# Optimization experiments

Measured on AMD Instinct MI355X. Metric: run time of the kernel, lower is better.

The kernel has to match this reference:

```python
import jax, jax.numpy as jnp
import numpy as np

E = 1024  # embedding_dim
A = 1024  # attention_dim


def setup_inputs() -> dict:
    key = jax.random.key(0)
    k0, k1, k2, k3 = jax.random.split(key, 4)
    embedded = jax.random.normal(k0, (4, 4096, E), dtype=jnp.float32)
    # torch Linear weight is [out, in]; stored here as [in, out] for x @ W
    scale = 1.0 / np.sqrt(E)
    Wk = jax.random.uniform(k1, (E, A), dtype=jnp.float32, minval=-scale, maxval=scale)
    Wq = jax.random.uniform(k2, (E, A), dtype=jnp.float32, minval=-scale, maxval=scale)
    Wv = jax.random.uniform(k3, (E, A), dtype=jnp.float32, minval=-scale, maxval=scale)
    return {"embedded": embedded, "Wk": Wk, "Wq": Wq, "Wv": Wv}


def reference(embedded, Wk, Wq, Wv):
    B, T, C = embedded.shape
    K = embedded @ Wk  # [B,T,A]
    Q = embedded @ Wq
    V = embedded @ Wv
    d_k = Q.shape[-1]
    scores = jnp.einsum('bqa,bka->bqk', Q, K) / jnp.sqrt(jnp.float32(d_k))
    causal = jnp.tril(jnp.ones((T, T), dtype=bool))
    scores = jnp.where(causal, scores, -jnp.inf)
    attn = jax.nn.softmax(scores, axis=-1)
    out = jnp.einsum('bqk,bka->bqa', attn, V)
    return jnp.round(out, decimals=4)
```

## Files before the change

### kernel.cpp

```cpp
#include <hip/hip_runtime.h>
#include <hip/hip_fp16.h>

#define T_SEQ 4096
#define NBATCH 4
#define EDIM 1024
#define ADIM 1024
#define MTOT (NBATCH * T_SEQ)

typedef _Float16 f16x8 __attribute__((ext_vector_type(8)));
typedef float f32x4 __attribute__((ext_vector_type(4)));

#define STAGE(SRC, LD, LDSARR)                                               \
  {                                                                          \
    _Pragma("unroll") for (int t = 0; t < 2; ++t) {                          \
      const int rb = w * 2 + t;                                              \
      const _Float16* gsrc =                                                 \
          (SRC) + (size_t)(rb * 16 + (lane & 15)) * (LD) + (lane >> 4) * 8;  \
      __builtin_amdgcn_global_load_lds(                                      \
          (const __attribute__((address_space(1))) void*)gsrc,               \
          (__attribute__((address_space(3))) void*)&LDSARR[rb * 512], 16,    \
          0, 0);                                                             \
    }                                                                        \
  }

#define FRAG(LDSARR, B4, G) (*(const f16x8*)&LDSARR[((B4) * 4 + (G)) * 128 + lr * 8])

__global__ __launch_bounds__(256) void cast_x(const float* __restrict__ X,
                                              _Float16* __restrict__ Xh) {
  const size_t i = ((size_t)blockIdx.x * 256 + threadIdx.x) * 8;
  float4 a = ((const float4*)(X + i))[0];
  float4 b = ((const float4*)(X + i))[1];
  f16x8 o = {(_Float16)a.x, (_Float16)a.y, (_Float16)a.z, (_Float16)a.w,
             (_Float16)b.x, (_Float16)b.y, (_Float16)b.z, (_Float16)b.w};
  *(f16x8*)(Xh + i) = o;
}

__global__ __launch_bounds__(256) void cast_transpose_w(
    const float* __restrict__ Wk, const float* __restrict__ Wq,
    const float* __restrict__ Wv, _Float16* __restrict__ Wt) {
  __shared__ float tile[32][33];
  const int z = blockIdx.z;
  const float* W = (z == 0) ? Wk : (z == 1) ? Wq : Wv;
  const int n0 = blockIdx.x * 32, k0 = blockIdx.y * 32;
  const int tx = threadIdx.x, ty = threadIdx.y;
#pragma unroll
  for (int yy = 0; yy < 32; yy += 8)
    tile[ty + yy][tx] = W[(size_t)(k0 + ty + yy) * ADIM + n0 + tx];
  __syncthreads();
  _Float16* out = Wt + (size_t)z * EDIM * ADIM;
#pragma unroll
  for (int yy = 0; yy < 32; yy += 8)
    out[(size_t)(n0 + ty + yy) * EDIM + k0 + tx] = (_Float16)tile[tx][ty + yy];
}

__global__ __launch_bounds__(256) void gemm_qkv(
    const _Float16* __restrict__ Xh, const _Float16* __restrict__ Wt,
    _Float16* __restrict__ Qb, _Float16* __restrict__ Kb,
    _Float16* __restrict__ Vt) {
  const int z = blockIdx.z;
  const _Float16* Bt = Wt + (size_t)z * EDIM * ADIM;
  __shared__ __align__(16) _Float16 Al[4096];
  __shared__ __align__(16) _Float16 Bl[4096];
  const int tid = threadIdx.x;
  const int lane = tid & 63, w = tid >> 6;
  const int wm = w >> 1, wn = w & 1;
  const int lr = lane & 15, g = lane >> 4;
  const int h = blockIdx.y * gridDim.x + blockIdx.x;
  const int orig = (h & 7) * 128 + (h >> 3);
  const int m0 = (orig >> 3) * 128, n0 = (orig & 7) * 128;

  f32x4 acc[4][4] = {};

  for (int k0 = 0; k0 < EDIM; k0 += 32) {
    STAGE(Xh + (size_t)m0 * EDIM + k0, EDIM, Al);
    STAGE(Bt + (size_t)n0 * EDIM + k0, EDIM, Bl);
    __syncthreads();
    f16x8 af[4], bf[4];
#pragma unroll
    for (int i = 0; i < 4; i++) af[i] = FRAG(Al, wm * 4 + i, g);
#pragma unroll
    for (int j = 0; j < 4; j++) bf[j] = FRAG(Bl, wn * 4 + j, g);
#pragma unroll
    for (int i = 0; i < 4; i++)
#pragma unroll
      for (int j = 0; j < 4; j++)
        acc[i][j] = __builtin_amdgcn_mfma_f32_16x16x32_f16(af[i], bf[j], acc[i][j], 0, 0, 0);
    __syncthreads();
  }

#pragma unroll
  for (int i = 0; i < 4; i++)
#pragma unroll
    for (int j = 0; j < 4; j++)
#pragma unroll
      for (int r = 0; r < 4; r++) {
        const int row = m0 + wm * 64 + i * 16 + 4 * g + r;
        const int col = n0 + wn * 64 + j * 16 + lr;
        const _Float16 hv = (_Float16)acc[i][j][r];
        if (z == 0)
          Kb[(size_t)row * ADIM + col] = hv;
        else if (z == 1)
          Qb[(size_t)row * ADIM + col] = hv;
        else {
          const int b = row >> 12, tt = row & 4095;
          Vt[((size_t)b * ADIM + col) * T_SEQ + tt] = hv;
        }
      }
}

__global__ __launch_bounds__(256) void gemm_sqk(
    const _Float16* __restrict__ Qb, const _Float16* __restrict__ Kb,
    _Float16* __restrict__ Sb) {
  __shared__ __align__(16) _Float16 Al[4096];
  __shared__ __align__(16) _Float16 Bl[4096];
  const int b = blockIdx.y;
  const int tid = threadIdx.x;
  const int lane = tid & 63, w = tid >> 6;
  const int wm = w >> 1, wn = w & 1;
  const int lr = lane & 15, g = lane >> 4;
  const int h = blockIdx.x;
  const int orig = (h & 7) * 66 + (h >> 3);
  int bi = (int)((sqrtf(8.f * orig + 1.f) - 1.f) * 0.5f);
  while ((bi + 1) * (bi + 2) / 2 <= orig) ++bi;
  while (bi * (bi + 1) / 2 > orig) --bi;
  const int bj = orig - bi * (bi + 1) / 2;
  const int m0 = bi * 128, n0 = bj * 128;
  const _Float16* A = Qb + (size_t)b * T_SEQ * ADIM;
  const _Float16* B = Kb + (size_t)b * T_SEQ * ADIM;

  f32x4 acc[4][4] = {};

  for (int k0 = 0; k0 < ADIM; k0 += 32) {
    STAGE(A + (size_t)m0 * ADIM + k0, ADIM, Al);
    STAGE(B + (size_t)n0 * ADIM + k0, ADIM, Bl);
    __syncthreads();
    f16x8 af[4], bf[4];
#pragma unroll
    for (int i = 0; i < 4; i++) af[i] = FRAG(Al, wm * 4 + i, g);
#pragma unroll
    for (int j = 0; j < 4; j++) bf[j] = FRAG(Bl, wn * 4 + j, g);
#pragma unroll
    for (int i = 0; i < 4; i++)
#pragma unroll
      for (int j = 0; j < 4; j++)
        acc[i][j] = __builtin_amdgcn_mfma_f32_16x16x32_f16(af[i], bf[j], acc[i][j], 0, 0, 0);
    __syncthreads();
  }

  _Float16* Srow = Sb + (size_t)b * T_SEQ * T_SEQ;
#pragma unroll
  for (int i = 0; i < 4; i++)
#pragma unroll
    for (int j = 0; j < 4; j++)
#pragma unroll
      for (int r = 0; r < 4; r++) {
        const int row = m0 + wm * 64 + i * 16 + 4 * g + r;
        const int col = n0 + wn * 64 + j * 16 + lr;
        Srow[(size_t)row * T_SEQ + col] = (_Float16)acc[i][j][r];
      }
}

__global__ __launch_bounds__(512) void softmax_rows(_Float16* __restrict__ S) {
  const int i = blockIdx.x, b = blockIdx.y;
  const int padded = ((i >> 7) + 1) << 7;
  const int tid = threadIdx.x;
  const int lane = tid & 63, w = tid >> 6;
  const int j0 = tid * 8;
  const bool active = j0 < padded;
  _Float16* row = S + ((size_t)b * T_SEQ + i) * T_SEQ;
  const float sm_scale = 0.03125f;

  float v[8];
  float m = -1e30f;
  if (active) {
    f16x8 x = *(const f16x8*)(row + j0);
#pragma unroll
    for (int jj = 0; jj < 8; jj++) {
      const float sv = (j0 + jj <= i) ? (float)x[jj] * sm_scale : -1e30f;
      v[jj] = sv;
      m = fmaxf(m, sv);
    }
  } else {
#pragma unroll
    for (int jj = 0; jj < 8; jj++) v[jj] = -1e30f;
  }
#pragma unroll
  for (int off = 1; off < 64; off <<= 1) m = fmaxf(m, __shfl_xor(m, off));
  __shared__ float redm[8], reds[8];
  if (lane == 0) redm[w] = m;
  __syncthreads();
#pragma unroll
  for (int ww = 0; ww < 8; ww++) m = fmaxf(m, redm[ww]);

  float s = 0.f;
#pragma unroll
  for (int jj = 0; jj < 8; jj++) {
    v[jj] = __expf(v[jj] - m);
    s += v[jj];
  }
#pragma unroll
  for (int off = 1; off < 64; off <<= 1) s += __shfl_xor(s, off);
  if (lane == 0) reds[w] = s;
  __syncthreads();
  s = 0.f;
#pragma unroll
  for (int ww = 0; ww < 8; ww++) s += reds[ww];
  const float inv = 1.f / s;

  if (active) {
    f16x8 o;
#pragma unroll
    for (int jj = 0; jj < 8; jj++) o[jj] = (_Float16)(v[jj] * inv);
    *(f16x8*)(row + j0) = o;
  }
}

__global__ __launch_bounds__(256) void gemm_pv(
    const _Float16* __restrict__ Pb, const _Float16* __restrict__ Vt,
    float* __restrict__ Out) {
  __shared__ __align__(16) _Float16 Al[4096];
  __shared__ __align__(16) _Float16 Bl[4096];
  const int b = blockIdx.y;
  const int tid = threadIdx.x;
  const int lane = tid & 63, w = tid >> 6;
  const int wm = w >> 1, wn = w & 1;
  const int lr = lane & 15, g = lane >> 4;
  const int h = blockIdx.x;
  const int orig = (h & 7) * 32 + (h >> 3);
  const int by = orig >> 3, bx = orig & 7;
  const int m0 = by * 128, n0 = bx * 128;
  const int kmax = (by + 1) * 128;
  const _Float16* A = Pb + (size_t)b * T_SEQ * T_SEQ;
  const _Float16* B = Vt + (size_t)b * ADIM * T_SEQ;

  f32x4 acc[4][4] = {};

  for (int k0 = 0; k0 < kmax; k0 += 32) {
    STAGE(A + (size_t)m0 * T_SEQ + k0, T_SEQ, Al);
    STAGE(B + (size_t)n0 * T_SEQ + k0, T_SEQ, Bl);
    __syncthreads();
    f16x8 af[4], bf[4];
#pragma unroll
    for (int i = 0; i < 4; i++) af[i] = FRAG(Al, wm * 4 + i, g);
#pragma unroll
    for (int j = 0; j < 4; j++) bf[j] = FRAG(Bl, wn * 4 + j, g);
#pragma unroll
    for (int i = 0; i < 4; i++)
#pragma unroll
      for (int j = 0; j < 4; j++)
        acc[i][j] = __builtin_amdgcn_mfma_f32_16x16x32_f16(af[i], bf[j], acc[i][j], 0, 0, 0);
    __syncthreads();
  }

#pragma unroll
  for (int i = 0; i < 4; i++)
#pragma unroll
    for (int j = 0; j < 4; j++)
#pragma unroll
      for (int r = 0; r < 4; r++) {
        const int row = m0 + wm * 64 + i * 16 + 4 * g + r;
        const int col = n0 + wn * 64 + j * 16 + lr;
        Out[((size_t)b * T_SEQ + row) * ADIM + col] = acc[i][j][r];
      }
}

extern "C" void kernel_launch(void* const* d_in, const int* in_sizes, int n_in,
                              void* d_out, int out_size, void* d_ws, size_t ws_size,
                              hipStream_t stream) {
  const float* X = (const float*)d_in[0];
  const float* Wk = (const float*)d_in[1];
  const float* Wq = (const float*)d_in[2];
  const float* Wv = (const float*)d_in[3];
  float* Out = (float*)d_out;

  char* ws = (char*)d_ws;
  const size_t WT_BYTES = (size_t)3 * EDIM * ADIM * 2;
  const size_t MAT_BYTES = (size_t)MTOT * ADIM * 2;
  _Float16* Wt = (_Float16*)ws;
  _Float16* Kb = (_Float16*)(ws + WT_BYTES);
  _Float16* Qb = (_Float16*)(ws + WT_BYTES + MAT_BYTES);
  _Float16* Vt = (_Float16*)(ws + WT_BYTES + 2 * MAT_BYTES);
  _Float16* Xh = (_Float16*)(ws + WT_BYTES + 3 * MAT_BYTES);
  _Float16* Sb = (_Float16*)(ws + WT_BYTES + 3 * MAT_BYTES);

  cast_x<<<dim3(MTOT * EDIM / 2048), dim3(256), 0, stream>>>(X, Xh);
  cast_transpose_w<<<dim3(32, 32, 3), dim3(32, 8), 0, stream>>>(Wk, Wq, Wv, Wt);
  gemm_qkv<<<dim3(8, 128, 3), dim3(256), 0, stream>>>(Xh, Wt, Qb, Kb, Vt);
  gemm_sqk<<<dim3(528, NBATCH), dim3(256), 0, stream>>>(Qb, Kb, Sb);
  softmax_rows<<<dim3(T_SEQ, NBATCH), dim3(512), 0, stream>>>(Sb);
  gemm_pv<<<dim3(256, NBATCH), dim3(256), 0, stream>>>(Sb, Vt, Out);
}
```

Measured before the change: 823.4 us.

## Split-K the causal PV GEMM for lower row blocks and reduce partials

Row blocks in the lower half of the causal P·V product have up to twice the K range of the upper ones, so those tiles become the long tail. They are now split into two K halves: one writes to the output and the other writes to a partial buffer that reuses the Q workspace. A new elementwise kernel then adds the partials into the output. This balances per-block work and raises the block count from 256 to 384 per batch, at the cost of an extra kernel launch and an extra read and write of half the output.

```diff
diff --git a/kernel.cpp b/kernel.cpp
--- a/kernel.cpp
+++ b/kernel.cpp
@@ -217,7 +217,7 @@
 
 __global__ __launch_bounds__(256) void gemm_pv(
     const _Float16* __restrict__ Pb, const _Float16* __restrict__ Vt,
-    float* __restrict__ Out) {
+    float* __restrict__ Part, float* __restrict__ Out) {
   __shared__ __align__(16) _Float16 Al[4096];
   __shared__ __align__(16) _Float16 Bl[4096];
   const int b = blockIdx.y;
@@ -226,16 +226,24 @@
   const int wm = w >> 1, wn = w & 1;
   const int lr = lane & 15, g = lane >> 4;
   const int h = blockIdx.x;
-  const int orig = (h & 7) * 32 + (h >> 3);
-  const int by = orig >> 3, bx = orig & 7;
+  const int orig = (h & 7) * 48 + (h >> 3);
+  int by, c, bx;
+  if (orig < 128) {
+    by = orig >> 3; c = 0; bx = orig & 7;
+  } else {
+    const int idx = orig - 128;
+    by = 16 + (idx >> 4); c = (idx >> 3) & 1; bx = idx & 7;
+  }
   const int m0 = by * 128, n0 = bx * 128;
+  const int kbeg = c * 2048;
   const int kmax = (by + 1) * 128;
+  const int kend = (c == 0) ? (kmax < 2048 ? kmax : 2048) : kmax;
   const _Float16* A = Pb + (size_t)b * T_SEQ * T_SEQ;
   const _Float16* B = Vt + (size_t)b * ADIM * T_SEQ;
 
   f32x4 acc[4][4] = {};
 
-  for (int k0 = 0; k0 < kmax; k0 += 32) {
+  for (int k0 = kbeg; k0 < kend; k0 += 32) {
     STAGE(A + (size_t)m0 * T_SEQ + k0, T_SEQ, Al);
     STAGE(B + (size_t)n0 * T_SEQ + k0, T_SEQ, Bl);
     __syncthreads();
@@ -260,8 +268,25 @@
       for (int r = 0; r < 4; r++) {
         const int row = m0 + wm * 64 + i * 16 + 4 * g + r;
         const int col = n0 + wn * 64 + j * 16 + lr;
-        Out[((size_t)b * T_SEQ + row) * ADIM + col] = acc[i][j][r];
+        if (c == 0)
+          Out[((size_t)b * T_SEQ + row) * ADIM + col] = acc[i][j][r];
+        else
+          Part[((size_t)b * 2048 + (row - 2048)) * ADIM + col] = acc[i][j][r];
       }
+}
+
+__global__ __launch_bounds__(256) void reduce_pv(const float* __restrict__ Part,
+                                                 float* __restrict__ Out) {
+  const size_t id = (size_t)blockIdx.x * 256 + threadIdx.x;
+  const int b = (int)(id >> 19);
+  const size_t rem = id & 524287;
+  const size_t row2 = rem >> 8, coli = rem & 255;
+  float4* o = (float4*)Out + ((size_t)(b * 4096 + 2048) + row2) * 256 + coli;
+  const float4* p = (const float4*)Part + ((size_t)b * 2048 + row2) * 256 + coli;
+  float4 ov = *o;
+  const float4 pv = *p;
+  ov.x += pv.x; ov.y += pv.y; ov.z += pv.z; ov.w += pv.w;
+  *o = ov;
 }
 
 extern "C" void kernel_launch(void* const* d_in, const int* in_sizes, int n_in,
@@ -282,11 +307,13 @@
   _Float16* Vt = (_Float16*)(ws + WT_BYTES + 2 * MAT_BYTES);
   _Float16* Xh = (_Float16*)(ws + WT_BYTES + 3 * MAT_BYTES);
   _Float16* Sb = (_Float16*)(ws + WT_BYTES + 3 * MAT_BYTES);
+  float* Part = (float*)Qb;
 
   cast_x<<<dim3(MTOT * EDIM / 2048), dim3(256), 0, stream>>>(X, Xh);
   cast_transpose_w<<<dim3(32, 32, 3), dim3(32, 8), 0, stream>>>(Wk, Wq, Wv, Wt);
   gemm_qkv<<<dim3(8, 128, 3), dim3(256), 0, stream>>>(Xh, Wt, Qb, Kb, Vt);
   gemm_sqk<<<dim3(528, NBATCH), dim3(256), 0, stream>>>(Qb, Kb, Sb);
   softmax_rows<<<dim3(T_SEQ, NBATCH), dim3(512), 0, stream>>>(Sb);
-  gemm_pv<<<dim3(256, NBATCH), dim3(256), 0, stream>>>(Sb, Vt, Out);
-}
+  gemm_pv<<<dim3(384, NBATCH), dim3(256), 0, stream>>>(Sb, Vt, Part, Out);
+  reduce_pv<<<dim3(NBATCH * 2048 * 1024 / 4 / 256), dim3(256), 0, stream>>>(Part, Out);
+}
```

Measured after the change: 695.0 us. 15.6% less time.
